# Optimization experiments

Measured on AMD Instinct MI355X. Metric: run time of the kernel, lower is better.

The kernel has to match this reference:

```python
import jax, jax.numpy as jnp
import numpy as np

D = 64          # data_size == latent_dim == noise_dim
DIM = 256       # sector_emb / attention width (hardcoded 256 in source)
H = 4           # heads (hardcoded via rearrange h=4)
N = D + 1       # tokens incl. cls
HIDDEN = 512
SECTORS = 11
B = 4096
E_DIM = N * DIM + DIM * DIM + DIM + DIM + 1  # 82689


def setup_inputs() -> dict:
    key = jax.random.key(0)
    ks = jax.random.split(key, 16)
    p = lambda k, shape: (jax.random.normal(k, shape, jnp.float32) * 0.02)
    return dict(
        X=jax.random.normal(ks[0], (B, D), jnp.float32),
        z=jax.random.normal(ks[1], (1, D), jnp.float32),
        sector=jax.random.randint(ks[2], (B, 1), 0, SECTORS),
        emb_table=p(ks[3], (SECTORS, DIM)),
        Wsp=p(ks[4], (D, DIM)), bsp=jnp.zeros((D,), jnp.float32),
        Wh=p(ks[5], (D, D)), bh=jnp.zeros((D,), jnp.float32),
        Wc=p(ks[6], (D, D)), bc=jnp.zeros((D,), jnp.float32),
        Wi=p(ks[7], (D, D)), bi=jnp.zeros((D,), jnp.float32),
        W_ih=p(ks[8], (4 * D, D)), W_hh=p(ks[9], (4 * D, D)),
        b_ih=jnp.zeros((4 * D,), jnp.float32), b_hh=jnp.zeros((4 * D,), jnp.float32),
        num_w=jax.random.normal(ks[10], (D, DIM), jnp.float32),
        num_b=jax.random.normal(ks[11], (D, DIM), jnp.float32),
        cls_token=jax.random.normal(ks[12], (1, 1, DIM), jnp.float32),
        W1=p(ks[13], (HIDDEN, D)), b1=jnp.zeros((HIDDEN,), jnp.float32),
        W2=p(ks[14], (E_DIM, HIDDEN)), b2=jnp.zeros((E_DIM,), jnp.float32),
    )


def reference(X, z, sector, emb_table, Wsp, bsp, Wh, bh, Wc, bc, Wi, bi,
              W_ih, W_hh, b_ih, b_hh, num_w, num_b, cls_token, W1, b1, W2, b2):
    # sector embedding + projection: s [B, D]
    s = emb_table[sector[:, 0]] @ Wsp.T + bsp

    # LSTM init (note source swaps names: h0 <- init_lin_h, c0 <- init_lin_c)
    h0 = jnp.tanh(z @ Wh.T + bh)
    c0 = jnp.tanh(z @ Wc.T + bc)
    inp = jnp.tanh(z @ Wi.T + bi)

    # single-step single-layer LSTM (seq len 1), PyTorch gate order i,f,g,o
    gates = inp @ W_ih.T + b_ih + h0 @ W_hh.T + b_hh
    i_g, f_g, g_g, o_g = jnp.split(gates, 4, axis=-1)
    c = jax.nn.sigmoid(f_g) * c0 + jax.nn.sigmoid(i_g) * jnp.tanh(g_g)
    h = jax.nn.sigmoid(o_g) * jnp.tanh(c)

    # hypernetwork: E [1, E_DIM]
    E = jax.nn.relu(h @ W1.T + b1) @ W2.T + b2
    e = E[0]
    a = N * DIM
    qw = e[:a].reshape(N, DIM)                  # q/k/v all use the same slice
    ow = e[a:a + DIM * DIM].reshape(DIM, DIM)
    ob = e[a + DIM * DIM:a + DIM * DIM + DIM]
    om = e[a + DIM * DIM + DIM:a + DIM * DIM + 2 * DIM].reshape(DIM, 1)
    outb = e[-1]

    # numerical embedding + cls token: Xt [B, N, DIM]
    Xs = X + s
    Xe = Xs[:, :, None] * num_w + num_b
    b = X.shape[0]
    Xt = jnp.concatenate([jnp.broadcast_to(cls_token, (b, 1, DIM)), Xe], axis=1)

    # per-token generated weights, then small MHA (dropout p=0.05 -> eval identity)
    hd = DIM // H
    scale = hd ** (-0.5)
    qkv = (Xt * qw).reshape(b, N, H, hd).transpose(0, 2, 1, 3)  # [B,H,N,hd]
    q = qkv * scale
    attn = jax.nn.softmax(jnp.einsum('bhid,bhjd->bhij', q, qkv), axis=-1)
    out = jnp.einsum('bhij,bhjd->bhid', attn, qkv)
    out = out.transpose(0, 2, 1, 3).reshape(b, N, DIM)

    out = jnp.einsum('bfi,ij->bfj', out, ow) + ob
    out = out + Xt
    out = jnp.einsum('bfi,ij->bfj', out, om) + outb  # [B, N, 1]
    return out[:, 0], attn
```

## Files before the change

kernel.cpp:

```cpp
#include <hip/hip_runtime.h>
#include <math.h>

#define D_ 64
#define DIM_ 256
#define NH_ 4
#define NN_ 65
#define SEC_ 11
#define B_ 4096
#define EDIM_ 82689

#define OFF_R       0
#define OFF_E       512
#define OFF_SALL    (OFF_E + 82944)
#define OFF_XS      (OFF_SALL + 704)
#define OFF_A       (OFF_XS + 262144)
#define OFF_C       (OFF_A + 16640)
#define OFF_AA      (OFF_C + 16640)
#define OFF_AC      (OFF_AA + 16900)
#define OFF_CC      (OFF_AC + 16900)
#define OFF_W2      (OFF_CC + 16900)
#define OFF_AW      (OFF_W2 + 256)
#define OFF_CW      (OFF_AW + 260)
#define OFF_CONST   (OFF_CW + 260)
#define OFF_PART    (OFF_CONST + 4)

__global__ __launch_bounds__(256) void kA(const float* __restrict__ z, const float* __restrict__ emb,
                        const float* __restrict__ Wsp, const float* __restrict__ bsp,
                        const float* __restrict__ Wh, const float* __restrict__ bh,
                        const float* __restrict__ Wc, const float* __restrict__ bc,
                        const float* __restrict__ Wi, const float* __restrict__ bi,
                        const float* __restrict__ W_ih, const float* __restrict__ W_hh,
                        const float* __restrict__ b_ih, const float* __restrict__ b_hh,
                        const float* __restrict__ W1, const float* __restrict__ b1,
                        float* __restrict__ ws) {
  __shared__ float sz[64], sh0[64], sc0[64], sinp[64], sgates[256], sh[64];
  int t = threadIdx.x;
  if (blockIdx.x == 0) {
    if (t < 64) sz[t] = z[t];
    __syncthreads();
    if (t < 192) {
      int d = t & 63; int which = t >> 6;
      const float* W = which == 0 ? Wh : (which == 1 ? Wc : Wi);
      const float* bv = which == 0 ? bh : (which == 1 ? bc : bi);
      float acc = bv[d];
      for (int k = 0; k < 64; ++k) acc = fmaf(sz[k], W[d * 64 + k], acc);
      float tv = tanhf(acc);
      if (which == 0) sh0[d] = tv; else if (which == 1) sc0[d] = tv; else sinp[d] = tv;
    }
    __syncthreads();
    {
      int g = t;
      float acc = b_ih[g] + b_hh[g];
      for (int k = 0; k < 64; ++k) acc = fmaf(sinp[k], W_ih[g * 64 + k], acc);
      for (int k = 0; k < 64; ++k) acc = fmaf(sh0[k], W_hh[g * 64 + k], acc);
      sgates[g] = acc;
    }
    __syncthreads();
    if (t < 64) {
      float ig = sgates[t], fg = sgates[64 + t], gg = sgates[128 + t], og = sgates[192 + t];
      float sf = 1.0f / (1.0f + expf(-fg));
      float si = 1.0f / (1.0f + expf(-ig));
      float so = 1.0f / (1.0f + expf(-og));
      float c = sf * sc0[t] + si * tanhf(gg);
      sh[t] = so * tanhf(c);
    }
    __syncthreads();
    for (int j = t; j < 512; j += 256) {
      float acc = b1[j];
      for (int k = 0; k < 64; ++k) acc = fmaf(sh[k], W1[j * 64 + k], acc);
      ws[OFF_R + j] = fmaxf(acc, 0.0f);
    }
  } else {
    int sec = blockIdx.x - 1;
    int lane = t & 63, wave = t >> 6;
    float e0 = emb[sec * 256 + lane];
    float e1 = emb[sec * 256 + 64 + lane];
    float e2 = emb[sec * 256 + 128 + lane];
    float e3 = emb[sec * 256 + 192 + lane];
    for (int dd = 0; dd < 16; ++dd) {
      int d = wave * 16 + dd;
      const float* wr = Wsp + d * 256;
      float acc = fmaf(wr[lane], e0,
                  fmaf(wr[64 + lane], e1,
                  fmaf(wr[128 + lane], e2, wr[192 + lane] * e3)));
      for (int off = 32; off; off >>= 1) acc += __shfl_xor(acc, off);
      if (lane == 0) ws[OFF_SALL + sec * 64 + d] = acc + bsp[d];
    }
  }
}

__global__ __launch_bounds__(256) void k2_E(const float* __restrict__ W2,
                                            const float* __restrict__ b2,
                                            const float* __restrict__ r,
                                            float* __restrict__ E) {
  int lane = threadIdx.x & 63;
  int wave = threadIdx.x >> 6;
  int row0 = (blockIdx.x * 4 + wave) * 8;
  float4 r0 = ((const float4*)r)[lane];
  float4 r1 = ((const float4*)r)[64 + lane];
  float acc[8];
  #pragma unroll
  for (int rr = 0; rr < 8; ++rr) {
    int row = row0 + rr;
    float4 w0 = make_float4(0.f, 0.f, 0.f, 0.f), w1 = w0;
    if (row < EDIM_) {
      const float4* w = (const float4*)(W2 + (size_t)row * 512);
      w0 = w[lane];
      w1 = w[64 + lane];
    }
    acc[rr] = w0.x * r0.x + w0.y * r0.y + w0.z * r0.z + w0.w * r0.w
            + w1.x * r1.x + w1.y * r1.y + w1.z * r1.z + w1.w * r1.w;
  }
  #pragma unroll
  for (int rr = 0; rr < 8; ++rr)
    for (int off = 32; off; off >>= 1) acc[rr] += __shfl_xor(acc[rr], off);
  #pragma unroll
  for (int rr = 0; rr < 8; ++rr) {
    int row = row0 + rr;
    if (row < EDIM_ && lane == rr) E[row] = acc[rr] + b2[row];
  }
}

__global__ __launch_bounds__(256) void kB(const float* __restrict__ E,
                                          const float* __restrict__ num_w,
                                          const float* __restrict__ num_b,
                                          const float* __restrict__ cls,
                                          float* __restrict__ ws) {
  __shared__ float red[256];
  int blk = blockIdx.x, t = threadIdx.x;
  float* A = ws + OFF_A;
  float* C = ws + OFF_C;
  if (blk < 65) {
    int j = blk, c = t;
    float qw = E[j * 256 + c];
    if (j == 0) {
      A[c] = 0.0f;
      C[c] = qw * cls[c];
    } else {
      A[j * 256 + c] = qw * num_w[(j - 1) * 256 + c];
      C[j * 256 + c] = qw * num_b[(j - 1) * 256 + c];
    }
  } else if (blk < 129) {
    int lane = t & 63, wave = t >> 6;
    int row = (blk - 65) * 4 + wave;
    const float* ow = E + 16640 + row * 256;
    const float* om = E + 82432;
    float acc = 0.0f;
    #pragma unroll
    for (int k = 0; k < 4; ++k) acc = fmaf(ow[k * 64 + lane], om[k * 64 + lane], acc);
    for (int off = 32; off; off >>= 1) acc += __shfl_xor(acc, off);
    if (lane == 0) ws[OFF_W2 + row] = acc;
  } else {
    red[t] = (E[82176 + t] + cls[t]) * E[82432 + t];
    __syncthreads();
    for (int s = 128; s; s >>= 1) {
      if (t < s) red[t] += red[t + s];
      __syncthreads();
    }
    if (t == 0) ws[OFF_CONST] = red[0] + E[82688];
  }
}

__global__ void k4_xs(const float* __restrict__ X, const int* __restrict__ sector,
                      const float* __restrict__ sall, float* __restrict__ Xs) {
  int idx = blockIdx.x * 256 + threadIdx.x;
  int b = idx >> 6, d = idx & 63;
  Xs[idx] = X[idx] + sall[sector[b] * 64 + d];
}

__global__ void k3b_coef(const float* __restrict__ A, const float* __restrict__ C,
                         const float* __restrict__ w2, float* __restrict__ AA,
                         float* __restrict__ AC, float* __restrict__ CC,
                         float* __restrict__ aw, float* __restrict__ cw) {
  int i = blockIdx.x;
  int h = blockIdx.y;
  __shared__ float sAi[64], sCi[64];
  int t = threadIdx.x;
  if (t < 64) {
    sAi[t] = A[i * 256 + h * 64 + t];
    sCi[t] = C[i * 256 + h * 64 + t];
  }
  __syncthreads();
  if (t < 65) {
    int j = t;
    const float* Aj = A + j * 256 + h * 64;
    const float* Cj = C + j * 256 + h * 64;
    float aa = 0.0f, ac = 0.0f, cc = 0.0f;
    for (int c = 0; c < 64; ++c) {
      float ajc = Aj[c], cjc = Cj[c];
      aa = fmaf(sAi[c], ajc, aa);
      ac = fmaf(sAi[c], cjc, ac);
      cc = fmaf(sCi[c], cjc, cc);
    }
    int base = h * 4225 + i * 65 + j;
    AA[base] = 0.125f * aa;
    AC[base] = 0.125f * ac;
    CC[base] = 0.125f * cc;
    if (i == 0) {
      const float* wh = w2 + h * 64;
      float a_ = 0.0f, c_ = 0.0f;
      for (int c = 0; c < 64; ++c) {
        a_ = fmaf(Aj[c], wh[c], a_);
        c_ = fmaf(Cj[c], wh[c], c_);
      }
      aw[h * 65 + j] = a_;
      cw[h * 65 + j] = c_;
    }
  }
}

#define MB_ 8
__global__ __launch_bounds__(256) void k5_attn(const float* __restrict__ ws,
                                               float* __restrict__ out,
                                               float* __restrict__ partial) {
  __shared__ float sAA[4225], sAC[4225], sCC[4225];
  __shared__ float sx[MB_ * 65], sinv[MB_ * 65], saw[65], scw[65];
  int t = threadIdx.x;
  int h = blockIdx.y;
  int b0 = blockIdx.x * MB_;
  const float* gAA = ws + OFF_AA + h * 4225;
  const float* gAC = ws + OFF_AC + h * 4225;
  const float* gCC = ws + OFF_CC + h * 4225;
  for (int idx = t; idx < 4225; idx += 256) {
    sAA[idx] = gAA[idx];
    sAC[idx] = gAC[idx];
    sCC[idx] = gCC[idx];
  }
  if (t < 65) {
    saw[t] = ws[OFF_AW + h * 65 + t];
    scw[t] = ws[OFF_CW + h * 65 + t];
  }
  const float* Xs = ws + OFF_XS;
  for (int idx = t; idx < MB_ * 64; idx += 256) {
    int bb = idx >> 6, d = idx & 63;
    sx[bb * 65 + 1 + d] = Xs[(size_t)(b0 + bb) * 64 + d];
  }
  if (t < MB_) sx[t * 65] = 0.0f;
  __syncthreads();
  int lane = t & 63, wave = t >> 6;

  for (int bb = wave; bb < MB_; bb += 4) {
    const float* xr = sx + bb * 65;
    float xi = xr[lane];
    float s = 0.0f;
    #pragma unroll 8
    for (int j = 0; j < 65; ++j) {
      float xj = xr[j];
      float aa = sAA[lane * 65 + j];
      float ac = sAC[lane * 65 + j];
      float act = sAC[j * 65 + lane];
      float cc = sCC[lane * 65 + j];
      float v = fmaf(xi, fmaf(xj, aa, ac), fmaf(xj, act, cc));
      s += __expf(v);
    }
    sinv[bb * 65 + lane] = 1.0f / s;
    {
      float x64 = xr[64];
      int j = lane;
      float xj = xr[j];
      float aa = sAA[64 * 65 + j];
      float ac = sAC[64 * 65 + j];
      float act = sAC[j * 65 + 64];
      float cc = sCC[64 * 65 + j];
      float e = __expf(fmaf(x64, fmaf(xj, aa, ac), fmaf(xj, act, cc)));
      for (int off = 32; off; off >>= 1) e += __shfl_xor(e, off);
      float aa4 = sAA[4224], ac4 = sAC[4224], cc4 = sCC[4224];
      e += __expf(fmaf(x64, fmaf(x64, aa4, ac4), fmaf(x64, ac4, cc4)));
      if (lane == 0) sinv[bb * 65 + 64] = 1.0f / e;
    }
  }
  __syncthreads();

  float xjv[MB_], x64v[MB_];
  #pragma unroll
  for (int bb = 0; bb < MB_; ++bb) {
    xjv[bb] = sx[bb * 65 + lane];
    x64v[bb] = sx[bb * 65 + 64];
  }
  for (int i = wave; i < 65; i += 4) {
    int j = lane;
    float aa = sAA[i * 65 + j];
    float ac = sAC[i * 65 + j];
    float act = sAC[j * 65 + i];
    float cc = sCC[i * 65 + j];
    float aa4 = sAA[i * 65 + 64];
    float ac4 = sAC[i * 65 + 64];
    float act4 = sAC[64 * 65 + i];
    float cc4 = sCC[i * 65 + 64];
    #pragma unroll
    for (int bb = 0; bb < MB_; ++bb) {
      float xi = sx[bb * 65 + i];
      float inv = sinv[bb * 65 + i];
      float xj = xjv[bb], x64 = x64v[bb];
      float e = __expf(fmaf(xi, fmaf(xj, aa, ac), fmaf(xj, act, cc))) * inv;
      float e4 = __expf(fmaf(xi, fmaf(x64, aa4, ac4), fmaf(x64, act4, cc4))) * inv;
      size_t obase = 4096 + (size_t)((b0 + bb) * NH_ + h) * 4225 + (size_t)i * 65;
      out[obase + j] = e;
      if (lane == 0) out[obase + 64] = e4;
      if (i == 0) {
        float p = e * fmaf(xj, saw[j], scw[j]);
        for (int off = 32; off; off >>= 1) p += __shfl_xor(p, off);
        p += e4 * fmaf(x64, saw[64], scw[64]);
        if (lane == 0) partial[(size_t)(b0 + bb) * NH_ + h] = p;
      }
    }
  }
}

__global__ void k6_final(const float* __restrict__ partial, const float* __restrict__ cst,
                         float* __restrict__ out) {
  int b = blockIdx.x * 256 + threadIdx.x;
  if (b < B_) {
    out[b] = partial[b * 4] + partial[b * 4 + 1] + partial[b * 4 + 2] + partial[b * 4 + 3]
           + cst[0];
  }
}

extern "C" void kernel_launch(void* const* d_in, const int* in_sizes, int n_in,
                              void* d_out, int out_size, void* d_ws, size_t ws_size,
                              hipStream_t stream) {
  const float* X     = (const float*)d_in[0];
  const float* z     = (const float*)d_in[1];
  const int*   sector= (const int*)d_in[2];
  const float* emb   = (const float*)d_in[3];
  const float* Wsp   = (const float*)d_in[4];
  const float* bsp   = (const float*)d_in[5];
  const float* Wh    = (const float*)d_in[6];
  const float* bh    = (const float*)d_in[7];
  const float* Wc    = (const float*)d_in[8];
  const float* bc    = (const float*)d_in[9];
  const float* Wi    = (const float*)d_in[10];
  const float* bi    = (const float*)d_in[11];
  const float* W_ih  = (const float*)d_in[12];
  const float* W_hh  = (const float*)d_in[13];
  const float* b_ih  = (const float*)d_in[14];
  const float* b_hh  = (const float*)d_in[15];
  const float* num_w = (const float*)d_in[16];
  const float* num_b = (const float*)d_in[17];
  const float* cls   = (const float*)d_in[18];
  const float* W1    = (const float*)d_in[19];
  const float* b1    = (const float*)d_in[20];
  const float* W2    = (const float*)d_in[21];
  const float* b2    = (const float*)d_in[22];
  float* ws  = (float*)d_ws;
  float* out = (float*)d_out;

  kA<<<12, 256, 0, stream>>>(z, emb, Wsp, bsp, Wh, bh, Wc, bc, Wi, bi,
                             W_ih, W_hh, b_ih, b_hh, W1, b1, ws);
  k4_xs<<<1024, 256, 0, stream>>>(X, sector, ws + OFF_SALL, ws + OFF_XS);
  k2_E<<<2585, 256, 0, stream>>>(W2, b2, ws + OFF_R, ws + OFF_E);
  kB<<<130, 256, 0, stream>>>(ws + OFF_E, num_w, num_b, cls, ws);
  dim3 g3b(65, 4);
  k3b_coef<<<g3b, 128, 0, stream>>>(ws + OFF_A, ws + OFF_C, ws + OFF_W2,
                                    ws + OFF_AA, ws + OFF_AC, ws + OFF_CC,
                                    ws + OFF_AW, ws + OFF_CW);
  dim3 g5(B_ / MB_, NH_);
  k5_attn<<<g5, 256, 0, stream>>>(ws, out, ws + OFF_PART);
  k6_final<<<16, 256, 0, stream>>>(ws + OFF_PART, ws + OFF_CONST, out);
}
```

Baseline: 539.3 us.

## Fuse Xs computation into attention kernel and compute softmax denominators inline

Removes the separate k4_xs kernel and its workspace buffer, computing X + sector projection directly while loading into shared memory in the attention kernel. The separate pre-pass that computed softmax row sums is removed. The denominator is now computed in the main loop by reducing exp values across the wave with shuffles, followed by normalization before the store. This saves one launch, a global round trip, and a duplicate pass of exponentials, at the cost of extra shuffle reductions and more registers per iteration.

```diff
diff --git a/kernel.cpp b/kernel.cpp
--- a/kernel.cpp
+++ b/kernel.cpp
@@ -12,8 +12,7 @@
 #define OFF_R       0
 #define OFF_E       512
 #define OFF_SALL    (OFF_E + 82944)
-#define OFF_XS      (OFF_SALL + 704)
-#define OFF_A       (OFF_XS + 262144)
+#define OFF_A       (OFF_SALL + 704)
 #define OFF_C       (OFF_A + 16640)
 #define OFF_AA      (OFF_C + 16640)
 #define OFF_AC      (OFF_AA + 16900)
@@ -161,13 +160,6 @@
   }
 }
 
-__global__ void k4_xs(const float* __restrict__ X, const int* __restrict__ sector,
-                      const float* __restrict__ sall, float* __restrict__ Xs) {
-  int idx = blockIdx.x * 256 + threadIdx.x;
-  int b = idx >> 6, d = idx & 63;
-  Xs[idx] = X[idx] + sall[sector[b] * 64 + d];
-}
-
 __global__ void k3b_coef(const float* __restrict__ A, const float* __restrict__ C,
                          const float* __restrict__ w2, float* __restrict__ AA,
                          float* __restrict__ AC, float* __restrict__ CC,
@@ -211,10 +203,12 @@
 
 #define MB_ 8
 __global__ __launch_bounds__(256) void k5_attn(const float* __restrict__ ws,
+                                               const float* __restrict__ X,
+                                               const int* __restrict__ sector,
                                                float* __restrict__ out,
                                                float* __restrict__ partial) {
   __shared__ float sAA[4225], sAC[4225], sCC[4225];
-  __shared__ float sx[MB_ * 65], sinv[MB_ * 65], saw[65], scw[65];
+  __shared__ float sx[MB_ * 65], saw[65], scw[65];
   int t = threadIdx.x;
   int h = blockIdx.y;
   int b0 = blockIdx.x * MB_;
@@ -230,46 +224,15 @@
     saw[t] = ws[OFF_AW + h * 65 + t];
     scw[t] = ws[OFF_CW + h * 65 + t];
   }
-  const float* Xs = ws + OFF_XS;
+  const float* sall = ws + OFF_SALL;
   for (int idx = t; idx < MB_ * 64; idx += 256) {
     int bb = idx >> 6, d = idx & 63;
-    sx[bb * 65 + 1 + d] = Xs[(size_t)(b0 + bb) * 64 + d];
+    int b = b0 + bb;
+    sx[bb * 65 + 1 + d] = X[(size_t)b * 64 + d] + sall[sector[b] * 64 + d];
   }
   if (t < MB_) sx[t * 65] = 0.0f;
   __syncthreads();
   int lane = t & 63, wave = t >> 6;
-
-  for (int bb = wave; bb < MB_; bb += 4) {
-    const float* xr = sx + bb * 65;
-    float xi = xr[lane];
-    float s = 0.0f;
-    #pragma unroll 8
-    for (int j = 0; j < 65; ++j) {
-      float xj = xr[j];
-      float aa = sAA[lane * 65 + j];
-      float ac = sAC[lane * 65 + j];
-      float act = sAC[j * 65 + lane];
-      float cc = sCC[lane * 65 + j];
-      float v = fmaf(xi, fmaf(xj, aa, ac), fmaf(xj, act, cc));
-      s += __expf(v);
-    }
-    sinv[bb * 65 + lane] = 1.0f / s;
-    {
-      float x64 = xr[64];
-      int j = lane;
-      float xj = xr[j];
-      float aa = sAA[64 * 65 + j];
-      float ac = sAC[64 * 65 + j];
-      float act = sAC[j * 65 + 64];
-      float cc = sCC[64 * 65 + j];
-      float e = __expf(fmaf(x64, fmaf(xj, aa, ac), fmaf(xj, act, cc)));
-      for (int off = 32; off; off >>= 1) e += __shfl_xor(e, off);
-      float aa4 = sAA[4224], ac4 = sAC[4224], cc4 = sCC[4224];
-      e += __expf(fmaf(x64, fmaf(x64, aa4, ac4), fmaf(x64, ac4, cc4)));
-      if (lane == 0) sinv[bb * 65 + 64] = 1.0f / e;
-    }
-  }
-  __syncthreads();
 
   float xjv[MB_], x64v[MB_];
   #pragma unroll
@@ -277,8 +240,8 @@
     xjv[bb] = sx[bb * 65 + lane];
     x64v[bb] = sx[bb * 65 + 64];
   }
+  int j = lane;
   for (int i = wave; i < 65; i += 4) {
-    int j = lane;
     float aa = sAA[i * 65 + j];
     float ac = sAC[i * 65 + j];
     float act = sAC[j * 65 + i];
@@ -287,20 +250,33 @@
     float ac4 = sAC[i * 65 + 64];
     float act4 = sAC[64 * 65 + i];
     float cc4 = sCC[i * 65 + 64];
+    float e[MB_], e4[MB_], s[MB_];
     #pragma unroll
     for (int bb = 0; bb < MB_; ++bb) {
       float xi = sx[bb * 65 + i];
-      float inv = sinv[bb * 65 + i];
       float xj = xjv[bb], x64 = x64v[bb];
-      float e = __expf(fmaf(xi, fmaf(xj, aa, ac), fmaf(xj, act, cc))) * inv;
-      float e4 = __expf(fmaf(xi, fmaf(x64, aa4, ac4), fmaf(x64, act4, cc4))) * inv;
+      e[bb] = __expf(fmaf(xi, fmaf(xj, aa, ac), fmaf(xj, act, cc)));
+      e4[bb] = __expf(fmaf(xi, fmaf(x64, aa4, ac4), fmaf(x64, act4, cc4)));
+      s[bb] = e[bb];
+    }
+    #pragma unroll
+    for (int off = 32; off; off >>= 1) {
+      #pragma unroll
+      for (int bb = 0; bb < MB_; ++bb) s[bb] += __shfl_xor(s[bb], off);
+    }
+    #pragma unroll
+    for (int bb = 0; bb < MB_; ++bb) {
+      float inv = 1.0f / (s[bb] + e4[bb]);
+      float p0 = e[bb] * inv;
+      float p4 = e4[bb] * inv;
       size_t obase = 4096 + (size_t)((b0 + bb) * NH_ + h) * 4225 + (size_t)i * 65;
-      out[obase + j] = e;
-      if (lane == 0) out[obase + 64] = e4;
+      out[obase + j] = p0;
+      if (lane == 0) out[obase + 64] = p4;
       if (i == 0) {
-        float p = e * fmaf(xj, saw[j], scw[j]);
+        float p = p0 * fmaf(xjv[bb], saw[j], scw[j]);
+        #pragma unroll
         for (int off = 32; off; off >>= 1) p += __shfl_xor(p, off);
-        p += e4 * fmaf(x64, saw[64], scw[64]);
+        p += p4 * fmaf(x64v[bb], saw[64], scw[64]);
         if (lane == 0) partial[(size_t)(b0 + bb) * NH_ + h] = p;
       }
     }
@@ -347,7 +323,6 @@
 
   kA<<<12, 256, 0, stream>>>(z, emb, Wsp, bsp, Wh, bh, Wc, bc, Wi, bi,
                              W_ih, W_hh, b_ih, b_hh, W1, b1, ws);
-  k4_xs<<<1024, 256, 0, stream>>>(X, sector, ws + OFF_SALL, ws + OFF_XS);
   k2_E<<<2585, 256, 0, stream>>>(W2, b2, ws + OFF_R, ws + OFF_E);
   kB<<<130, 256, 0, stream>>>(ws + OFF_E, num_w, num_b, cls, ws);
   dim3 g3b(65, 4);
@@ -355,6 +330,6 @@
                                     ws + OFF_AA, ws + OFF_AC, ws + OFF_CC,
                                     ws + OFF_AW, ws + OFF_CW);
   dim3 g5(B_ / MB_, NH_);
-  k5_attn<<<g5, 256, 0, stream>>>(ws, out, ws + OFF_PART);
+  k5_attn<<<g5, 256, 0, stream>>>(ws, X, sector, out, ws + OFF_PART);
   k6_final<<<16, 256, 0, stream>>>(ws + OFF_PART, ws + OFF_CONST, out);
 }
```

New measurement: 529.3 us. About the same (-1.9%).
